# Kernel tuning notes

Hardware: AMD Instinct MI355X
Metric: run time of the kernel (lower is better)

Reference implementation:

```python
import jax, jax.numpy as jnp
import numpy as np

B, N, C = 2, 2048, 1024
H, D = 16, 64          # num_heads, head_dim
FF = 4096              # mlp hidden = 4*C
EPS = 1e-5


def layernorm(x, g, b):
    mu = jnp.mean(x, axis=-1, keepdims=True)
    var = jnp.mean((x - mu) ** 2, axis=-1, keepdims=True)
    return (x - mu) * jax.lax.rsqrt(var + EPS) * g + b


def setup_inputs() -> dict:
    key = jax.random.key(0)
    ks = jax.random.split(key, 8)
    s = lambda d: 1.0 / np.sqrt(d)
    return {
        "x": jax.random.normal(ks[0], (B, N, C), jnp.float32),
        "ln1_g": jnp.ones((C,), jnp.float32),
        "ln1_b": jnp.zeros((C,), jnp.float32),
        "qkv_w": jax.random.normal(ks[1], (3 * C, C), jnp.float32) * s(C),
        "proj_w": jax.random.normal(ks[2], (C, C), jnp.float32) * s(C),
        "proj_b": jnp.zeros((C,), jnp.float32),
        "ln2_g": jnp.ones((C,), jnp.float32),
        "ln2_b": jnp.zeros((C,), jnp.float32),
        "w1": jax.random.normal(ks[3], (FF, C), jnp.float32) * s(C),
        "b1": jnp.zeros((FF,), jnp.float32),
        "w2": jax.random.normal(ks[4], (C, FF), jnp.float32) * s(FF),
        "b2": jnp.zeros((C,), jnp.float32),
    }


def reference(x, ln1_g, ln1_b, qkv_w, proj_w, proj_b, ln2_g, ln2_b, w1, b1, w2, b2):
    # ---- attention sub-block ----
    h = layernorm(x, ln1_g, ln1_b)                       # [B,N,C]
    qkv = h @ qkv_w.T                                    # [B,N,3C]
    qkv = qkv.reshape(B, N, 3, H, D).transpose(2, 0, 3, 1, 4)  # [3,B,H,N,D]
    q, k, v = qkv[0], qkv[1], qkv[2]
    scale = D ** -0.5
    attn = jnp.einsum("bhnd,bhmd->bhnm", q, k) * scale   # [B,H,N,N]
    attn = jax.nn.softmax(attn, axis=-1)
    ao = jnp.einsum("bhnm,bhmd->bhnd", attn, v)          # [B,H,N,D]
    ao = ao.transpose(0, 2, 1, 3).reshape(B, N, C)
    x = x + ao @ proj_w.T + proj_b
    # ---- MLP sub-block ----
    h2 = layernorm(x, ln2_g, ln2_b)
    mlp = jax.nn.gelu(h2 @ w1.T + b1, approximate=False) @ w2.T + b2
    return x + mlp
```

## Files before the change

### kernel.cpp

```cpp
#include <hip/hip_runtime.h>
#include <hip/hip_bf16.h>

typedef __hip_bfloat16 obf;
typedef __attribute__((ext_vector_type(8))) __bf16 bf16x8;
typedef __attribute__((ext_vector_type(4))) float f32x4;

#define DEVINL __device__ __forceinline__

DEVINL void gload_lds16(const void* g, void* l) {
  __builtin_amdgcn_global_load_lds((const __attribute__((address_space(1))) void*)g,
                                   (__attribute__((address_space(3))) void*)l,
                                   16, 0, 0);
}

__global__ void __launch_bounds__(256) f2b_kernel(const float* __restrict__ in,
                                                  __bf16* __restrict__ out, int n8)
{
  const int i = blockIdx.x * 256 + threadIdx.x;
  if (i >= n8) return;
  const float4 a = ((const float4*)in)[i * 2];
  const float4 b = ((const float4*)in)[i * 2 + 1];
  bf16x8 o;
  o[0] = (__bf16)a.x; o[1] = (__bf16)a.y; o[2] = (__bf16)a.z; o[3] = (__bf16)a.w;
  o[4] = (__bf16)b.x; o[5] = (__bf16)b.y; o[6] = (__bf16)b.z; o[7] = (__bf16)b.w;
  ((bf16x8*)out)[i] = o;
}

__global__ void __launch_bounds__(256) ln_f2b_kernel(
    const float* __restrict__ xin, const float* __restrict__ g, const float* __restrict__ b,
    obf* __restrict__ lnout, const float* __restrict__ win, __bf16* __restrict__ wout,
    int nln, int n8)
{
  __shared__ float red[8];
  const int t = threadIdx.x;
  if ((int)blockIdx.x < nln) {
    const int row = blockIdx.x;
    const int lane = t & 63, w = t >> 6;
    float4 f = ((const float4*)xin)[(size_t)row * 256 + t];
    float v[4] = { f.x, f.y, f.z, f.w };
    float s1 = v[0] + v[1] + v[2] + v[3];
    float s2 = v[0]*v[0] + v[1]*v[1] + v[2]*v[2] + v[3]*v[3];
    #pragma unroll
    for (int off = 32; off >= 1; off >>= 1) {
      s1 += __shfl_xor(s1, off);
      s2 += __shfl_xor(s2, off);
    }
    if (lane == 0) { red[w] = s1; red[4 + w] = s2; }
    __syncthreads();
    s1 = red[0] + red[1] + red[2] + red[3];
    s2 = red[4] + red[5] + red[6] + red[7];
    const float mu = s1 * (1.f / 1024.f);
    const float var = s2 * (1.f / 1024.f) - mu * mu;
    const float rs = rsqrtf(var + 1e-5f);
    const float4 gv = ((const float4*)g)[t];
    const float4 bv = ((const float4*)b)[t];
    obf* op = lnout + (size_t)row * 1024 + t * 4;
    op[0] = __float2bfloat16((v[0] - mu) * rs * gv.x + bv.x);
    op[1] = __float2bfloat16((v[1] - mu) * rs * gv.y + bv.y);
    op[2] = __float2bfloat16((v[2] - mu) * rs * gv.z + bv.z);
    op[3] = __float2bfloat16((v[3] - mu) * rs * gv.w + bv.w);
  } else {
    const int i = (blockIdx.x - nln) * 256 + t;
    if (i >= n8) return;
    const float4 a = ((const float4*)win)[i * 2];
    const float4 b2 = ((const float4*)win)[i * 2 + 1];
    bf16x8 o;
    o[0] = (__bf16)a.x;  o[1] = (__bf16)a.y;  o[2] = (__bf16)a.z;  o[3] = (__bf16)a.w;
    o[4] = (__bf16)b2.x; o[5] = (__bf16)b2.y; o[6] = (__bf16)b2.z; o[7] = (__bf16)b2.w;
    ((bf16x8*)wout)[i] = o;
  }
}

enum { EPI_NONE = 0, EPI_BIAS_RES_F32OUT = 1, EPI_BIAS_GELU = 2, EPI_BIAS_RESF32_F32OUT = 3 };

template<int EPI, int NI>
__global__ void __launch_bounds__(256, 2) gemm_bt(
    const obf* __restrict__ A, const obf* __restrict__ Bw,
    void* __restrict__ Cout, const float* __restrict__ bias,
    const void* __restrict__ resid, int M, int N, int K)
{
  __shared__ __align__(16) char As[128 * 64 * 2];
  __shared__ __align__(16) char Bs[NI * 32 * 64 * 2];
  const int tid = threadIdx.x;
  const int lane = tid & 63;
  const int w = tid >> 6, wr = w >> 1, wc = w & 1;
  const int bm = blockIdx.y * 128, bn = blockIdx.x * (NI * 32);
  const size_t lda = (size_t)K * 2;

  f32x4 acc[4][NI];
  #pragma unroll
  for (int i = 0; i < 4; i++)
    #pragma unroll
    for (int j = 0; j < NI; j++) {
      acc[i][j][0] = 0.f; acc[i][j][1] = 0.f; acc[i][j][2] = 0.f; acc[i][j][3] = 0.f;
    }

  for (int k0 = 0; k0 < K; k0 += 64) {
    #pragma unroll
    for (int i = 0; i < 4; i++) {
      const int ci = tid + 256 * i;
      const int r = ci >> 3;
      const int gb = ((ci & 7) * 16) ^ ((r & 7) << 4);
      gload_lds16((const char*)A + (size_t)(bm + r) * lda + (size_t)k0 * 2 + gb, As + ci * 16);
    }
    #pragma unroll
    for (int i = 0; i < NI; i++) {
      const int ci = tid + 256 * i;
      const int r = ci >> 3;
      const int gb = ((ci & 7) * 16) ^ ((r & 7) << 4);
      gload_lds16((const char*)Bw + (size_t)(bn + r) * lda + (size_t)k0 * 2 + gb, Bs + ci * 16);
    }
    __syncthreads();

    bf16x8 af[4][2], bfr[NI][2];
    #pragma unroll
    for (int mi = 0; mi < 4; mi++) {
      const int r = wr * 64 + mi * 16 + (lane & 15);
      #pragma unroll
      for (int ks = 0; ks < 2; ks++) {
        const int cb = ks * 64 + ((lane >> 4) * 16);
        af[mi][ks] = *(const bf16x8*)(As + r * 128 + (cb ^ ((r & 7) << 4)));
      }
    }
    #pragma unroll
    for (int ni = 0; ni < NI; ni++) {
      const int r = wc * (NI * 16) + ni * 16 + (lane & 15);
      #pragma unroll
      for (int ks = 0; ks < 2; ks++) {
        const int cb = ks * 64 + ((lane >> 4) * 16);
        bfr[ni][ks] = *(const bf16x8*)(Bs + r * 128 + (cb ^ ((r & 7) << 4)));
      }
    }
    #pragma unroll
    for (int ks = 0; ks < 2; ks++)
      #pragma unroll
      for (int mi = 0; mi < 4; mi++)
        #pragma unroll
        for (int ni = 0; ni < NI; ni++)
          acc[mi][ni] = __builtin_amdgcn_mfma_f32_16x16x32_bf16(af[mi][ks], bfr[ni][ks], acc[mi][ni], 0, 0, 0);
    __syncthreads();
  }

  #pragma unroll
  for (int mi = 0; mi < 4; mi++) {
    #pragma unroll
    for (int ni = 0; ni < NI; ni++) {
      const int col = bn + wc * (NI * 16) + ni * 16 + (lane & 15);
      float bv = 0.f;
      if (EPI != EPI_NONE) bv = bias[col];
      #pragma unroll
      for (int r = 0; r < 4; r++) {
        const int row = bm + wr * 64 + mi * 16 + ((lane >> 4) << 2) + r;
        const float vacc = acc[mi][ni][r];
        const size_t idx = (size_t)row * N + col;
        if (EPI == EPI_NONE) {
          ((obf*)Cout)[idx] = __float2bfloat16(vacc);
        } else if (EPI == EPI_BIAS_RES_F32OUT) {
          const float x0 = ((const float*)resid)[idx];
          ((float*)Cout)[idx] = vacc + bv + x0;
        } else if (EPI == EPI_BIAS_GELU) {
          const float u = vacc + bv;
          const float e = exp2f(-2.30218709f * (u + 0.044715f * u * u * u));
          ((obf*)Cout)[idx] = __float2bfloat16(u / (1.f + e));
        } else {
          const float x0 = ((const float*)resid)[idx];
          ((float*)Cout)[idx] = vacc + bv + x0;
        }
      }
    }
  }
}

__global__ void __launch_bounds__(256) vtrans_kernel(const obf* __restrict__ qkv, obf* __restrict__ vt)
{
  const int bh = blockIdx.y;
  const int b = bh >> 4, h = bh & 15;
  const int n0 = blockIdx.x * 64;
  __shared__ __bf16 tile[64][72];
  const int t = threadIdx.x;
  {
    const int n = t >> 2;
    const int c0 = (t & 3) * 16;
    const __bf16* src = (const __bf16*)qkv + ((size_t)(b * 2048 + n0 + n)) * 3072 + 2048 + h * 64 + c0;
    bf16x8 u0 = *(const bf16x8*)src;
    bf16x8 u1 = *(const bf16x8*)(src + 8);
    #pragma unroll
    for (int j = 0; j < 8; j++) { tile[n][c0 + j] = u0[j]; tile[n][c0 + 8 + j] = u1[j]; }
  }
  __syncthreads();
  {
    const int d = t >> 2;
    const int c0 = (t & 3) * 16;
    bf16x8 o0, o1;
    #pragma unroll
    for (int j = 0; j < 8; j++) { o0[j] = tile[c0 + j][d]; o1[j] = tile[c0 + 8 + j][d]; }
    __bf16* dst = (__bf16*)vt + ((size_t)bh * 64 + d) * 2048 + n0 + c0;
    *(bf16x8*)dst = o0;
    *(bf16x8*)(dst + 8) = o1;
  }
}

__global__ void __launch_bounds__(512, 2) attn_kernel(
    const obf* __restrict__ qkv_, const obf* __restrict__ vt_, obf* __restrict__ ao)
{
  const __bf16* qkv = (const __bf16*)qkv_;
  const __bf16* vt  = (const __bf16*)vt_;
  const int bid = blockIdx.x;
  const int xcd = bid & 7, idx = bid >> 3;
  const int bh = xcd * 4 + (idx >> 4);
  const int q0 = (idx & 15) * 128;
  const int b = bh >> 4, h = bh & 15;
  const int tid = threadIdx.x, lane = tid & 63, w = tid >> 6;
  const int l15 = lane & 15, hi = lane >> 4;

  __shared__ __align__(16) char Ks[2][64 * 128];
  __shared__ __align__(16) char Vs[2][64 * 128];
  __shared__ __align__(16) char Ps[8 * 16 * 128];

  bf16x8 qf[2];
  {
    const int qrow = q0 + w * 16 + l15;
    #pragma unroll
    for (int ks = 0; ks < 2; ks++)
      qf[ks] = *(const bf16x8*)(qkv + ((size_t)(b * 2048 + qrow)) * 3072 + h * 64 + ks * 32 + hi * 8);
  }

  f32x4 o[4];
  #pragma unroll
  for (int j = 0; j < 4; j++) { o[j][0]=0.f; o[j][1]=0.f; o[j][2]=0.f; o[j][3]=0.f; }
  float lrow[4] = { 0.f, 0.f, 0.f, 0.f };

  const float kfac = 0.125f * 1.44269504089f;

  const int kr = tid >> 3, kc = (tid & 7) * 8;
  const int kcb = (tid & 7) * 16;
  const int kswz = kcb ^ ((kr & 7) << 4);

  bf16x8 pk, pv;
  pk = *(const bf16x8*)(qkv + ((size_t)(b * 2048 + kr)) * 3072 + 1024 + h * 64 + kc);
  pv = *(const bf16x8*)(vt + ((size_t)bh * 64 + kr) * 2048 + kc);
  *(bf16x8*)(Ks[0] + kr * 128 + kswz) = pk;
  *(bf16x8*)(Vs[0] + kr * 128 + kswz) = pv;
  __syncthreads();

  for (int kt = 0; kt < 2048; kt += 64) {
    const int cur = (kt >> 6) & 1;
    if (kt + 64 < 2048) {
      pk = *(const bf16x8*)(qkv + ((size_t)(b * 2048 + kt + 64 + kr)) * 3072 + 1024 + h * 64 + kc);
      pv = *(const bf16x8*)(vt + ((size_t)bh * 64 + kr) * 2048 + kt + 64 + kc);
    }

    f32x4 s[4];
    #pragma unroll
    for (int j = 0; j < 4; j++) { s[j][0]=0.f; s[j][1]=0.f; s[j][2]=0.f; s[j][3]=0.f; }
    #pragma unroll
    for (int ni = 0; ni < 4; ni++) {
      const int r = ni * 16 + l15;
      const bf16x8 kf0 = *(const bf16x8*)(Ks[cur] + r * 128 + ((hi * 16) ^ ((r & 7) << 4)));
      const bf16x8 kf1 = *(const bf16x8*)(Ks[cur] + r * 128 + ((64 + hi * 16) ^ ((r & 7) << 4)));
      s[ni] = __builtin_amdgcn_mfma_f32_16x16x32_bf16(qf[0], kf0, s[ni], 0, 0, 0);
      s[ni] = __builtin_amdgcn_mfma_f32_16x16x32_bf16(qf[1], kf1, s[ni], 0, 0, 0);
    }

    #pragma unroll
    for (int r = 0; r < 4; r++) {
      const int qrl = (hi << 2) + r;
      char* psrow = Ps + w * 2048 + qrl * 128;
      float psum = 0.f;
      #pragma unroll
      for (int ni = 0; ni < 4; ni++) {
        const float p = exp2f(s[ni][r] * kfac);
        psum += p;
        *(__bf16*)(psrow + (((ni * 16 + l15) * 2) ^ ((qrl & 7) << 4))) = (__bf16)p;
      }
      lrow[r] += psum;
    }

    #pragma unroll
    for (int ks = 0; ks < 2; ks++) {
      const int rr = l15;
      const bf16x8 pa = *(const bf16x8*)(Ps + w * 2048 + rr * 128 + (((ks * 32 + hi * 8) * 2) ^ ((rr & 7) << 4)));
      #pragma unroll
      for (int df = 0; df < 4; df++) {
        const int dr = df * 16 + l15;
        const int cb = (ks * 32 + hi * 8) * 2;
        const bf16x8 vb = *(const bf16x8*)(Vs[cur] + dr * 128 + (cb ^ ((dr & 7) << 4)));
        o[df] = __builtin_amdgcn_mfma_f32_16x16x32_bf16(pa, vb, o[df], 0, 0, 0);
      }
    }

    if (kt + 64 < 2048) {
      *(bf16x8*)(Ks[cur ^ 1] + kr * 128 + kswz) = pk;
      *(bf16x8*)(Vs[cur ^ 1] + kr * 128 + kswz) = pv;
    }
    __syncthreads();
  }

  #pragma unroll
  for (int r = 0; r < 4; r++) {
    lrow[r] += __shfl_xor(lrow[r], 1);
    lrow[r] += __shfl_xor(lrow[r], 2);
    lrow[r] += __shfl_xor(lrow[r], 4);
    lrow[r] += __shfl_xor(lrow[r], 8);
  }
  #pragma unroll
  for (int r = 0; r < 4; r++) {
    const float inv = 1.f / lrow[r];
    const int qrow = q0 + w * 16 + (hi << 2) + r;
    #pragma unroll
    for (int df = 0; df < 4; df++) {
      const int col = h * 64 + df * 16 + l15;
      ao[((size_t)(b * 2048 + qrow)) * 1024 + col] = __float2bfloat16(o[df][r] * inv);
    }
  }
}

extern "C" void kernel_launch(void* const* d_in, const int* in_sizes, int n_in,
                              void* d_out, int out_size, void* d_ws, size_t ws_size,
                              hipStream_t stream) {
  const float* x      = (const float*)d_in[0];
  const float* ln1_g  = (const float*)d_in[1];
  const float* ln1_b  = (const float*)d_in[2];
  const float* qkv_w  = (const float*)d_in[3];
  const float* proj_w = (const float*)d_in[4];
  const float* proj_b = (const float*)d_in[5];
  const float* ln2_g  = (const float*)d_in[6];
  const float* ln2_b  = (const float*)d_in[7];
  const float* w1     = (const float*)d_in[8];
  const float* b1     = (const float*)d_in[9];
  const float* w2     = (const float*)d_in[10];
  const float* b2     = (const float*)d_in[11];
  float* out = (float*)d_out;

  char* ws = (char*)d_ws;
  float* x2   = (float*)ws;
  obf*   h    = (obf*)(ws + (16u << 20));
  obf*   qkv  = (obf*)(ws + (24u << 20));
  obf*   ao   = (obf*)(ws + (48u << 20));
  obf*   m1   = (obf*)(ws + (24u << 20));
  __bf16* slot = (__bf16*)(ws + (56u << 20));
  __bf16* wb_w2 = (__bf16*)(ws + (16u << 20));

  const int M = 4096;

  ln_f2b_kernel<<<M + 1536, 256, 0, stream>>>(x, ln1_g, ln1_b, h,
                                              qkv_w, slot, M, 3072 * 1024 / 8);
  gemm_bt<EPI_NONE, 4><<<dim3(3072 / 128, M / 128), 256, 0, stream>>>(
      h, (const obf*)slot, qkv, nullptr, nullptr, M, 3072, 1024);
  vtrans_kernel<<<dim3(32, 32), 256, 0, stream>>>(qkv, (obf*)slot);
  attn_kernel<<<512, 512, 0, stream>>>(qkv, (const obf*)slot, ao);
  f2b_kernel<<<(1024 * 1024 / 8 + 255) / 256, 256, 0, stream>>>(proj_w, slot, 1024 * 1024 / 8);
  gemm_bt<EPI_BIAS_RES_F32OUT, 2><<<dim3(1024 / 64, M / 128), 256, 0, stream>>>(
      ao, (const obf*)slot, x2, proj_b, x, M, 1024, 1024);
  ln_f2b_kernel<<<M + 2048, 256, 0, stream>>>(x2, ln2_g, ln2_b, h,
                                              w1, slot, M, 4096 * 1024 / 8);
  gemm_bt<EPI_BIAS_GELU, 4><<<dim3(4096 / 128, M / 128), 256, 0, stream>>>(
      h, (const obf*)slot, m1, b1, nullptr, M, 4096, 1024);
  f2b_kernel<<<(4096 * 1024 / 8 + 255) / 256, 256, 0, stream>>>(w2, wb_w2, 4096 * 1024 / 8);
  gemm_bt<EPI_BIAS_RESF32_F32OUT, 2><<<dim3(1024 / 64, M / 128), 256, 0, stream>>>(
      m1, (const obf*)wb_w2, out, b2, x2, M, 1024, 4096);
}
```

Before: 243.0 us.

## Fold V transpose into attention LDS staging and merge proj weight conversion

Removes the separate V-transpose kernel. The attention kernel now reads V rows straight from the qkv buffer and scatters them transposed into swizzled LDS using scalar bf16 stores. The proj_w fp32-to-bf16 conversion is also folded into the first LN/convert launch, which removes a separate kernel launch. The cost is eight 2-byte LDS stores per thread per tile in place of one 16-byte store, which risks LDS bank conflicts and more store instructions in the attention loop.

```diff
diff --git a/kernel.cpp b/kernel.cpp
--- a/kernel.cpp
+++ b/kernel.cpp
@@ -26,15 +26,18 @@
   ((bf16x8*)out)[i] = o;
 }
 
-__global__ void __launch_bounds__(256) ln_f2b_kernel(
+__global__ void __launch_bounds__(256) ln_f2b2_kernel(
     const float* __restrict__ xin, const float* __restrict__ g, const float* __restrict__ b,
-    obf* __restrict__ lnout, const float* __restrict__ win, __bf16* __restrict__ wout,
-    int nln, int n8)
+    obf* __restrict__ lnout,
+    const float* __restrict__ win1, __bf16* __restrict__ wout1, int n8_1, int nb1,
+    const float* __restrict__ win2, __bf16* __restrict__ wout2, int n8_2,
+    int nln)
 {
   __shared__ float red[8];
   const int t = threadIdx.x;
-  if ((int)blockIdx.x < nln) {
-    const int row = blockIdx.x;
+  const int bx = blockIdx.x;
+  if (bx < nln) {
+    const int row = bx;
     const int lane = t & 63, w = t >> 6;
     float4 f = ((const float4*)xin)[(size_t)row * 256 + t];
     float v[4] = { f.x, f.y, f.z, f.w };
@@ -59,15 +62,24 @@
     op[1] = __float2bfloat16((v[1] - mu) * rs * gv.y + bv.y);
     op[2] = __float2bfloat16((v[2] - mu) * rs * gv.z + bv.z);
     op[3] = __float2bfloat16((v[3] - mu) * rs * gv.w + bv.w);
-  } else {
-    const int i = (blockIdx.x - nln) * 256 + t;
-    if (i >= n8) return;
-    const float4 a = ((const float4*)win)[i * 2];
-    const float4 b2 = ((const float4*)win)[i * 2 + 1];
+  } else if (bx < nln + nb1) {
+    const int i = (bx - nln) * 256 + t;
+    if (i >= n8_1) return;
+    const float4 a = ((const float4*)win1)[i * 2];
+    const float4 b2 = ((const float4*)win1)[i * 2 + 1];
     bf16x8 o;
     o[0] = (__bf16)a.x;  o[1] = (__bf16)a.y;  o[2] = (__bf16)a.z;  o[3] = (__bf16)a.w;
     o[4] = (__bf16)b2.x; o[5] = (__bf16)b2.y; o[6] = (__bf16)b2.z; o[7] = (__bf16)b2.w;
-    ((bf16x8*)wout)[i] = o;
+    ((bf16x8*)wout1)[i] = o;
+  } else {
+    const int i = (bx - nln - nb1) * 256 + t;
+    if (i >= n8_2) return;
+    const float4 a = ((const float4*)win2)[i * 2];
+    const float4 b2 = ((const float4*)win2)[i * 2 + 1];
+    bf16x8 o;
+    o[0] = (__bf16)a.x;  o[1] = (__bf16)a.y;  o[2] = (__bf16)a.z;  o[3] = (__bf16)a.w;
+    o[4] = (__bf16)b2.x; o[5] = (__bf16)b2.y; o[6] = (__bf16)b2.z; o[7] = (__bf16)b2.w;
+    ((bf16x8*)wout2)[i] = o;
   }
 }
 
@@ -171,40 +183,10 @@
   }
 }
 
-__global__ void __launch_bounds__(256) vtrans_kernel(const obf* __restrict__ qkv, obf* __restrict__ vt)
-{
-  const int bh = blockIdx.y;
-  const int b = bh >> 4, h = bh & 15;
-  const int n0 = blockIdx.x * 64;
-  __shared__ __bf16 tile[64][72];
-  const int t = threadIdx.x;
-  {
-    const int n = t >> 2;
-    const int c0 = (t & 3) * 16;
-    const __bf16* src = (const __bf16*)qkv + ((size_t)(b * 2048 + n0 + n)) * 3072 + 2048 + h * 64 + c0;
-    bf16x8 u0 = *(const bf16x8*)src;
-    bf16x8 u1 = *(const bf16x8*)(src + 8);
-    #pragma unroll
-    for (int j = 0; j < 8; j++) { tile[n][c0 + j] = u0[j]; tile[n][c0 + 8 + j] = u1[j]; }
-  }
-  __syncthreads();
-  {
-    const int d = t >> 2;
-    const int c0 = (t & 3) * 16;
-    bf16x8 o0, o1;
-    #pragma unroll
-    for (int j = 0; j < 8; j++) { o0[j] = tile[c0 + j][d]; o1[j] = tile[c0 + 8 + j][d]; }
-    __bf16* dst = (__bf16*)vt + ((size_t)bh * 64 + d) * 2048 + n0 + c0;
-    *(bf16x8*)dst = o0;
-    *(bf16x8*)(dst + 8) = o1;
-  }
-}
-
 __global__ void __launch_bounds__(512, 2) attn_kernel(
-    const obf* __restrict__ qkv_, const obf* __restrict__ vt_, obf* __restrict__ ao)
+    const obf* __restrict__ qkv_, obf* __restrict__ ao)
 {
   const __bf16* qkv = (const __bf16*)qkv_;
-  const __bf16* vt  = (const __bf16*)vt_;
   const int bid = blockIdx.x;
   const int xcd = bid & 7, idx = bid >> 3;
   const int bh = xcd * 4 + (idx >> 4);
@@ -238,16 +220,20 @@
 
   bf16x8 pk, pv;
   pk = *(const bf16x8*)(qkv + ((size_t)(b * 2048 + kr)) * 3072 + 1024 + h * 64 + kc);
-  pv = *(const bf16x8*)(vt + ((size_t)bh * 64 + kr) * 2048 + kc);
+  pv = *(const bf16x8*)(qkv + ((size_t)(b * 2048 + kr)) * 3072 + 2048 + h * 64 + kc);
   *(bf16x8*)(Ks[0] + kr * 128 + kswz) = pk;
-  *(bf16x8*)(Vs[0] + kr * 128 + kswz) = pv;
+  #pragma unroll
+  for (int j = 0; j < 8; j++) {
+    const int d = kc + j;
+    *(__bf16*)(Vs[0] + d * 128 + ((kr * 2) ^ ((d & 7) << 4))) = pv[j];
+  }
   __syncthreads();
 
   for (int kt = 0; kt < 2048; kt += 64) {
     const int cur = (kt >> 6) & 1;
     if (kt + 64 < 2048) {
       pk = *(const bf16x8*)(qkv + ((size_t)(b * 2048 + kt + 64 + kr)) * 3072 + 1024 + h * 64 + kc);
-      pv = *(const bf16x8*)(vt + ((size_t)bh * 64 + kr) * 2048 + kt + 64 + kc);
+      pv = *(const bf16x8*)(qkv + ((size_t)(b * 2048 + kt + 64 + kr)) * 3072 + 2048 + h * 64 + kc);
     }
 
     f32x4 s[4];
@@ -291,7 +277,11 @@
 
     if (kt + 64 < 2048) {
       *(bf16x8*)(Ks[cur ^ 1] + kr * 128 + kswz) = pk;
-      *(bf16x8*)(Vs[cur ^ 1] + kr * 128 + kswz) = pv;
+      #pragma unroll
+      for (int j = 0; j < 8; j++) {
+        const int d = kc + j;
+        *(__bf16*)(Vs[cur ^ 1] + d * 128 + ((kr * 2) ^ ((d & 7) << 4))) = pv[j];
+      }
     }
     __syncthreads();
   }
@@ -338,24 +328,28 @@
   obf*   qkv  = (obf*)(ws + (24u << 20));
   obf*   ao   = (obf*)(ws + (48u << 20));
   obf*   m1   = (obf*)(ws + (24u << 20));
-  __bf16* slot = (__bf16*)(ws + (56u << 20));
-  __bf16* wb_w2 = (__bf16*)(ws + (16u << 20));
+  __bf16* wb_qkv  = (__bf16*)(ws + (56u << 20));
+  __bf16* wb_proj = (__bf16*)(ws + (62u << 20));
+  __bf16* wb_w1   = (__bf16*)(ws + (56u << 20));
+  __bf16* wb_w2   = (__bf16*)(ws + (16u << 20));
 
   const int M = 4096;
 
-  ln_f2b_kernel<<<M + 1536, 256, 0, stream>>>(x, ln1_g, ln1_b, h,
-                                              qkv_w, slot, M, 3072 * 1024 / 8);
+  ln_f2b2_kernel<<<M + 1536 + 512, 256, 0, stream>>>(
+      x, ln1_g, ln1_b, h,
+      qkv_w, wb_qkv, 3072 * 1024 / 8, 1536,
+      proj_w, wb_proj, 1024 * 1024 / 8, M);
   gemm_bt<EPI_NONE, 4><<<dim3(3072 / 128, M / 128), 256, 0, stream>>>(
-      h, (const obf*)slot, qkv, nullptr, nullptr, M, 3072, 1024);
-  vtrans_kernel<<<dim3(32, 32), 256, 0, stream>>>(qkv, (obf*)slot);
-  attn_kernel<<<512, 512, 0, stream>>>(qkv, (const obf*)slot, ao);
-  f2b_kernel<<<(1024 * 1024 / 8 + 255) / 256, 256, 0, stream>>>(proj_w, slot, 1024 * 1024 / 8);
+      h, (const obf*)wb_qkv, qkv, nullptr, nullptr, M, 3072, 1024);
+  attn_kernel<<<512, 512, 0, stream>>>(qkv, ao);
   gemm_bt<EPI_BIAS_RES_F32OUT, 2><<<dim3(1024 / 64, M / 128), 256, 0, stream>>>(
-      ao, (const obf*)slot, x2, proj_b, x, M, 1024, 1024);
-  ln_f2b_kernel<<<M + 2048, 256, 0, stream>>>(x2, ln2_g, ln2_b, h,
-                                              w1, slot, M, 4096 * 1024 / 8);
+      ao, (const obf*)wb_proj, x2, proj_b, x, M, 1024, 1024);
+  ln_f2b2_kernel<<<M + 2048, 256, 0, stream>>>(
+      x2, ln2_g, ln2_b, h,
+      w1, wb_w1, 4096 * 1024 / 8, 2048,
+      nullptr, nullptr, 0, M);
   gemm_bt<EPI_BIAS_GELU, 4><<<dim3(4096 / 128, M / 128), 256, 0, stream>>>(
-      h, (const obf*)slot, m1, b1, nullptr, M, 4096, 1024);
+      h, (const obf*)wb_w1, m1, b1, nullptr, M, 4096, 1024);
   f2b_kernel<<<(4096 * 1024 / 8 + 255) / 256, 256, 0, stream>>>(w2, wb_w2, 4096 * 1024 / 8);
   gemm_bt<EPI_BIAS_RESF32_F32OUT, 2><<<dim3(1024 / 64, M / 128), 256, 0, stream>>>(
       m1, (const obf*)wb_w2, out, b2, x2, M, 1024, 4096);
```

Result: slower. 250.3 us (+3.0%).
